# Kernel tuning notes

Measured on AMD Instinct MI355X. Metric: run time of the kernel, lower is better.

The kernel has to match this reference:

```python
import jax, jax.numpy as jnp
import numpy as np

N, IN, HID, OUT, HD = 512, 256, 256, 256, 64  # n_agents, in_dim, hid_dim, out_dim, head_dim (out_dim // n_heads)


def _mlp2(x, w1, b1, w2, b2):
    return jax.nn.relu(x @ w1.T + b1) @ w2.T + b2


def setup_inputs():
    key = jax.random.key(0)
    ks = jax.random.split(key, 32)
    p = lambda i, shape: jax.random.normal(ks[i], shape, dtype=jnp.float32) * 0.05
    V = jax.random.normal(ks[0], (N, IN), dtype=jnp.float32)
    adj = jax.random.randint(ks[1], (N, N), 0, 2, dtype=jnp.int32)
    adj = adj.at[jnp.arange(N), jnp.arange(N)].set(1)  # self-loops so no softmax row is all -inf
    prev_hidden = jax.random.normal(ks[2], (N, HID), dtype=jnp.float32)
    return {
        "V": V, "adj": adj, "prev_hidden": prev_hidden,
        "W1": p(3, (HID, IN)), "sa0": p(4, (HID,)), "sa1": p(5, (HID,)),
        "ce_w1": p(6, (HID, 2 * IN)), "ce_b1": p(7, (HID,)), "ce_w2": p(8, (HD, HID)), "ce_b2": p(9, (HD,)),
        "ca0": p(10, (HD,)), "ca1": p(11, (HD,)),
        "te_w1": p(12, (HID, IN + HID)), "te_b1": p(13, (HID,)), "te_w2": p(14, (HD, HID)), "te_b2": p(15, (HD,)),
        "ta0": p(16, (HD,)), "ta1": p(17, (HD,)),
        "pe_w1": p(18, (HID, 3 * IN)), "pe_b1": p(19, (HID,)), "pe_w2": p(20, (HD, HID)), "pe_b2": p(21, (HD,)),
        "pa0": p(22, (HD,)), "pa1": p(23, (HD,)),
        "W2": p(24, (OUT, HID + 2 * HD + 1)), "op_w": p(25, (OUT, OUT)), "op_b": p(26, (OUT,)),
        "ln_g": jnp.ones((OUT,), jnp.float32), "ln_b": jnp.zeros((OUT,), jnp.float32),
    }


def _forward(V, adj, prev_hidden, W1, sa0, sa1, ce_w1, ce_b1, ce_w2, ce_b2, ca0, ca1,
             te_w1, te_b1, te_w2, te_b2, ta0, ta1, pe_w1, pe_b1, pe_w2, pe_b2, pa0, pa1,
             W2, op_w, op_b, ln_g, ln_b):
    neg = -jnp.inf
    # --- branch 1: standard GAT attention ---
    Wh1 = V @ W1.T                                             # (N, HID)
    s1 = (Wh1 @ sa0)[:, None] + (Wh1 @ sa1)[None, :]           # (N, N)
    s1 = jnp.where(adj == 0, neg, s1)
    H1 = jax.nn.softmax(s1, axis=1) @ Wh1                      # (N, HID)
    # --- branch 2: causal, all ordered pairs i != j ---
    wA, wB = ce_w1[:, :IN], ce_w1[:, IN:]
    h = jax.nn.relu((V @ wA.T)[:, None, :] + (V @ wB.T)[None, :, :] + ce_b1)  # (N, N, HID)
    f = h @ ce_w2.T + ce_b2                                    # (N, N, HD)
    s2 = jnp.where(jnp.eye(N, dtype=bool), neg, f @ (ca0 + ca1))
    a2 = jax.nn.softmax(s2.reshape(-1)).reshape(N, N)          # softmax over all off-diagonal pairs
    H2 = jnp.broadcast_to(jnp.einsum('ij,ijd->d', a2, f), (N, HD))
    # --- branch 3: temporal; (N,1) scores broadcast against (N,N) causal mask ---
    tf = _mlp2(jnp.concatenate([V, prev_hidden], -1), te_w1, te_b1, te_w2, te_b2)  # (N, HD)
    ts = tf @ (ta0 + ta1)                                      # (N,)
    cmask = jnp.triu(jnp.ones((N, N), dtype=bool), 1)
    s3 = jnp.where(cmask, neg, jnp.broadcast_to(ts[:, None], (N, N)))
    H3 = jax.nn.softmax(s3, axis=1) @ tf                       # (N, HD) == prefix means of tf
    # --- branch 4: cooperative; first two neighbors in index order (zeros if < 2) ---
    pos = jnp.where(adj == 1, jnp.arange(N)[None, :], N)
    srt = jnp.sort(pos, axis=1)
    i0, i1 = srt[:, 0], srt[:, 1]
    valid = (i1 < N)[:, None]
    n0 = jnp.where(valid, V[jnp.clip(i0, 0, N - 1)], 0.0)
    n1 = jnp.where(valid, V[jnp.clip(i1, 0, N - 1)], 0.0)
    cf = _mlp2(jnp.concatenate([V, n0, n1], -1), pe_w1, pe_b1, pe_w2, pe_b2)  # (N, HD)
    # torch: softmax over dim of size 1 -> all ones, alpha^T @ cf == column sums -> (HD,)
    # then unsqueezed to (HD,1) and zero-padded to (N,1) since HD < N  (faithful to source bug)
    H4v = cf.sum(axis=0)
    H4 = jnp.concatenate([H4v, jnp.zeros((N - HD,), V.dtype)])[:, None]       # (N, 1)
    # --- combine ---
    Hc = jnp.concatenate([H1, H2, H3, H4], axis=-1) @ W2.T     # (N, OUT)
    out = Hc @ op_w.T + op_b
    mu = out.mean(-1, keepdims=True)
    var = ((out - mu) ** 2).mean(-1, keepdims=True)
    y = (out - mu) / jnp.sqrt(var + 1e-5) * ln_g + ln_b        # LayerNorm, eps=1e-5
    return jax.nn.elu(y)                                       # dropout is identity in eval


def reference(V, adj, prev_hidden, W1, sa0, sa1, ce_w1, ce_b1, ce_w2, ce_b2, ca0, ca1,
              te_w1, te_b1, te_w2, te_b2, ta0, ta1, pe_w1, pe_b1, pe_w2, pe_b2, pa0, pa1,
              W2, op_w, op_b, ln_g, ln_b):
    return _forward(V, adj, prev_hidden, W1, sa0, sa1, ce_w1, ce_b1, ce_w2, ce_b2, ca0, ca1,
                    te_w1, te_b1, te_w2, te_b2, ta0, ta1, pe_w1, pe_b1, pe_w2, pe_b2, pa0, pa1,
                    W2, op_w, op_b, ln_g, ln_b)
```

## Files before the change

### kernel.cpp

```cpp
#include <hip/hip_runtime.h>

typedef unsigned short u16;

constexpr int kN   = 512;
constexpr int kIN  = 256;
constexpr int kHID = 256;
constexpr int kHD  = 64;
constexpr int kOUT = 256;

__device__ __forceinline__ float us2f(u16 u){
  union { unsigned int i; float f; } c; c.i = ((unsigned int)u) << 16; return c.f;
}
__device__ __forceinline__ u16 f2us(float f){
  union { float f; unsigned int i; } c; c.f = f;
  unsigned int r = c.i + 0x7fff + ((c.i >> 16) & 1);
  return (u16)(r >> 16);
}
__device__ __forceinline__ float ldraw(const void* p, size_t i, bool f32){
  return f32 ? ((const float*)p)[i] : us2f(((const u16*)p)[i]);
}

__device__ bool probe_is_f32(const unsigned int* __restrict__ V){
  __shared__ int cnt;
  if (threadIdx.x == 0) cnt = 0;
  __syncthreads();
  int c = 0;
  for (int k = threadIdx.x; k < 4096; k += 256){
    float x = us2f((u16)(V[k] & 0xffffu));
    if (!(fabsf(x) <= 32.0f)) c++;
  }
  atomicAdd(&cnt, c);
  __syncthreads();
  return cnt > 64;
}

__device__ __forceinline__ float blk_red(float v, float* tmp, bool isMax){
  int lane = threadIdx.x & 63, wv = threadIdx.x >> 6;
  #pragma unroll
  for (int o = 32; o > 0; o >>= 1){
    float t = __shfl_down(v, o, 64);
    v = isMax ? fmaxf(v, t) : (v + t);
  }
  __syncthreads();
  if (lane == 0) tmp[wv] = v;
  __syncthreads();
  float r = tmp[0];
  for (int i = 1; i < 4; ++i) r = isMax ? fmaxf(r, tmp[i]) : (r + tmp[i]);
  return r;
}

constexpr int kNConv = 22;
struct ConvArgs { const void* src[kNConv]; float* dst[kNConv]; int n[kNConv]; };
struct GSeg2 { const float* X; const float* W; float* C; int ldx, ldw, ldc, K;
               const float* bias; int act; };
struct GS32 { const float* X; const float* W; float* C; int ldx, ldw, ldc, K; int bkn; };

struct Args {
  const unsigned int* Vraw;
  const int* adj;
  const void* rprev;
  int* flag; void* out;
  const void *rca0,*rca1,*rcw2,*rcb2,*rtw2,*rpw2;
  float *Vf,*W1f,*sa1f,*cw1f,*cb1f,*cw2f,*cb2f,*ca0f,*ca1f;
  float *tw1f,*tb1f,*tw2f,*tb2f,*pw1f,*pb1f,*pw2f,*pb2f;
  float *W2f,*opwf,*opbf,*lngf,*lnbf;
  float *tw2t,*pw2t,*Wcomb,*OM,*ow4;
  float *Wh1,*e1v,*wadj,*Hc,*Am,*Bm,*uvec,*beta;
  float *s2,*maxp,*zp,*MZ,*gsum;
  float *hidden_t,*hidden_p,*tfm,*cfm,*H4v,*Xp,*Xt,*out3;
  ConvArgs ca;
  GSeg2 gs[5];
};

__device__ __forceinline__ void gemm32_body(const GS32 sg, int tm, int tn, int tid,
                                            float* Xs, float* Ws)
{
  const int i0 = tm << 5, n0 = tn << 5;
  const int xrow = tid >> 3;
  const int xk = (tid & 7) << 2;
  const int rg = (tid >> 4) << 1;
  const int cg = (tid & 15) << 1;
  const float* Xb = sg.X + (size_t)i0 * sg.ldx;
  const float* Wb = sg.bkn ? (sg.W + n0) : (sg.W + (size_t)n0 * sg.ldw);
  float4 xr, wr;
  auto loadT = [&](int kt){
    xr = *(const float4*)(Xb + (size_t)xrow * sg.ldx + kt + xk);
    if (sg.bkn) wr = *(const float4*)(Wb + (size_t)(kt + xrow) * sg.ldw + xk);
    else        wr = *(const float4*)(Wb + (size_t)xrow * sg.ldw + kt + xk);
  };
  auto writeT = [&](int bu){
    float* xs = Xs + bu*1152;
    xs[(xk+0)*36 + xrow] = xr.x; xs[(xk+1)*36 + xrow] = xr.y;
    xs[(xk+2)*36 + xrow] = xr.z; xs[(xk+3)*36 + xrow] = xr.w;
    float* wsp = Ws + bu*1152;
    if (sg.bkn){
      wsp[xrow*36 + xk+0] = wr.x; wsp[xrow*36 + xk+1] = wr.y;
      wsp[xrow*36 + xk+2] = wr.z; wsp[xrow*36 + xk+3] = wr.w;
    } else {
      wsp[(xk+0)*36 + xrow] = wr.x; wsp[(xk+1)*36 + xrow] = wr.y;
      wsp[(xk+2)*36 + xrow] = wr.z; wsp[(xk+3)*36 + xrow] = wr.w;
    }
  };
  loadT(0); writeT(0); __syncthreads();
  float a00=0,a01=0,a10=0,a11=0;
  const int nkt = sg.K >> 5;
  for (int t = 0; t < nkt; ++t){
    if (t+1 < nkt) loadT((t+1) << 5);
    const float* xs = Xs + (t&1)*1152;
    const float* wsp = Ws + (t&1)*1152;
    #pragma unroll
    for (int kk = 0; kk < 32; ++kk){
      float2 av = *(const float2*)&xs[kk*36 + rg];
      float2 bv = *(const float2*)&wsp[kk*36 + cg];
      a00 += av.x*bv.x; a01 += av.x*bv.y;
      a10 += av.y*bv.x; a11 += av.y*bv.y;
    }
    if (t+1 < nkt) writeT((t+1)&1);
    __syncthreads();
  }
  float* cp = sg.C + (size_t)(i0+rg)*sg.ldc + n0 + cg;
  *(float2*)cp = make_float2(a00, a01);
  *(float2*)(cp + sg.ldc) = make_float2(a10, a11);
}

__device__ void body_gemmA(const Args& A, int it, int tid, char* SM)
{
  float (*Xs)[32][68] = (float (*)[32][68])SM;
  float (*Ws)[32][68] = (float (*)[32][68])(SM + 17408);
  int seg = it >> 5, x = it & 31;
  const GSeg2 sg = A.gs[seg];
  const int tm = x & 7, tn = x >> 3;
  const int i0 = tm << 6, n0 = tn << 6;

  const int xrow = tid >> 3;
  const int xk   = (tid & 7) << 2;
  const int rg = (tid >> 4) << 2;
  const int cg = (tid & 15) << 2;

  const float* Xb = sg.X + (size_t)i0 * sg.ldx;
  const float* Wb = sg.W + (size_t)n0 * sg.ldw;

  float4 xr0, xr1, wr0, wr1;
  auto loadT = [&](int kt){
    xr0 = *(const float4*)(Xb + (size_t)xrow * sg.ldx + kt + xk);
    xr1 = *(const float4*)(Xb + (size_t)(xrow+32) * sg.ldx + kt + xk);
    wr0 = *(const float4*)(Wb + (size_t)xrow * sg.ldw + kt + xk);
    wr1 = *(const float4*)(Wb + (size_t)(xrow+32) * sg.ldw + kt + xk);
  };
  auto writeT = [&](int bu){
    Xs[bu][xk+0][xrow] = xr0.x;  Xs[bu][xk+1][xrow] = xr0.y;
    Xs[bu][xk+2][xrow] = xr0.z;  Xs[bu][xk+3][xrow] = xr0.w;
    Xs[bu][xk+0][xrow+32] = xr1.x;  Xs[bu][xk+1][xrow+32] = xr1.y;
    Xs[bu][xk+2][xrow+32] = xr1.z;  Xs[bu][xk+3][xrow+32] = xr1.w;
    Ws[bu][xk+0][xrow]    = wr0.x; Ws[bu][xk+1][xrow]    = wr0.y;
    Ws[bu][xk+2][xrow]    = wr0.z; Ws[bu][xk+3][xrow]    = wr0.w;
    Ws[bu][xk+0][xrow+32] = wr1.x; Ws[bu][xk+1][xrow+32] = wr1.y;
    Ws[bu][xk+2][xrow+32] = wr1.z; Ws[bu][xk+3][xrow+32] = wr1.w;
  };

  loadT(0); writeT(0); __syncthreads();

  float acc[4][4] = {};
  const int nkt = sg.K >> 5;
  for (int t = 0; t < nkt; ++t){
    if (t + 1 < nkt) loadT((t + 1) << 5);
    const int bu = t & 1;
    #pragma unroll
    for (int kk = 0; kk < 32; ++kk){
      const float4 av = *(const float4*)&Xs[bu][kk][rg];
      const float4 bv = *(const float4*)&Ws[bu][kk][cg];
      acc[0][0]+=av.x*bv.x; acc[0][1]+=av.x*bv.y; acc[0][2]+=av.x*bv.z; acc[0][3]+=av.x*bv.w;
      acc[1][0]+=av.y*bv.x; acc[1][1]+=av.y*bv.y; acc[1][2]+=av.y*bv.z; acc[1][3]+=av.y*bv.w;
      acc[2][0]+=av.z*bv.x; acc[2][1]+=av.z*bv.y; acc[2][2]+=av.z*bv.z; acc[2][3]+=av.z*bv.w;
      acc[3][0]+=av.w*bv.x; acc[3][1]+=av.w*bv.y; acc[3][2]+=av.w*bv.z; acc[3][3]+=av.w*bv.w;
    }
    if (t + 1 < nkt) writeT((t + 1) & 1);
    __syncthreads();
  }

  float bb[4] = {0.f, 0.f, 0.f, 0.f};
  if (sg.bias){
    bb[0] = sg.bias[n0+cg+0]; bb[1] = sg.bias[n0+cg+1];
    bb[2] = sg.bias[n0+cg+2]; bb[3] = sg.bias[n0+cg+3];
  }
  #pragma unroll
  for (int ri = 0; ri < 4; ++ri){
    float4 v = make_float4(acc[ri][0]+bb[0], acc[ri][1]+bb[1],
                           acc[ri][2]+bb[2], acc[ri][3]+bb[3]);
    if (sg.act){
      v.x = fmaxf(v.x, 0.f); v.y = fmaxf(v.y, 0.f);
      v.z = fmaxf(v.z, 0.f); v.w = fmaxf(v.w, 0.f);
    }
    *(float4*)(sg.C + (size_t)(i0 + rg + ri) * sg.ldc + (n0 + cg)) = v;
  }

  if (seg == 0){
    int cb = n0 + cg;
    float s0 = A.sa1f[cb], s1 = A.sa1f[cb+1], s2v = A.sa1f[cb+2], s3 = A.sa1f[cb+3];
    #pragma unroll
    for (int ri = 0; ri < 4; ++ri){
      float v = acc[ri][0]*s0 + acc[ri][1]*s1 + acc[ri][2]*s2v + acc[ri][3]*s3;
      v += __shfl_xor(v, 1, 16);
      v += __shfl_xor(v, 2, 16);
      v += __shfl_xor(v, 4, 16);
      v += __shfl_xor(v, 8, 16);
      if ((tid & 15) == 0) atomicAdd(&A.e1v[i0 + rg + ri], v);
    }
  }
}

__global__ __launch_bounds__(256) void k_s0(Args A)
{
  __shared__ __align__(16) char SM[16896];
  int it = blockIdx.x, tid = threadIdx.x;
  bool f32 = probe_is_f32(A.Vraw);
  if (it < 256){
    if (it == 0){
      if (tid == 0) *A.flag = f32 ? 1 : 0;
      A.e1v[tid] = 0.f; A.e1v[tid + 256] = 0.f;
    }
    int t = it*256 + tid;
    for (int s = 0; s < kNConv; ++s){
      int n4 = A.ca.n[s] >> 2;
      float4* d = (float4*)A.ca.dst[s];
      if (f32){
        const float4* sf = (const float4*)A.ca.src[s];
        for (int i = t; i < n4; i += 65536) d[i] = sf[i];
      } else {
        const ushort4* sb = (const ushort4*)A.ca.src[s];
        for (int i = t; i < n4; i += 65536){
          ushort4 u = sb[i];
          d[i] = make_float4(us2f(u.x), us2f(u.y), us2f(u.z), us2f(u.w));
        }
      }
    }
  } else if (it < 768){
    unsigned long long* msk = (unsigned long long*)SM;
    int* sj = (int*)(SM + 64);
    int i = it - 256;
    int w = tid >> 6, lane = tid & 63;
    unsigned long long m0 = __ballot(A.adj[(size_t)i*kN + tid] != 0);
    unsigned long long m1 = __ballot(A.adj[(size_t)i*kN + 256 + tid] != 0);
    if (lane == 0){ msk[w] = m0; msk[4 + w] = m1; }
    __syncthreads();
    if (tid == 0){
      int j0 = -1, j1 = -1;
      for (int c = 0; c < 8 && j1 < 0; ++c){
        unsigned long long m = msk[c];
        while (m && j1 < 0){
          int bb = __builtin_ctzll(m);
          int j = c*64 + bb;
          if (j0 < 0) j0 = j; else j1 = j;
          m &= m - 1;
        }
      }
      if (j1 < 0) j0 = -1;
      sj[0] = j0; sj[1] = j1;
    }
    __syncthreads();
    int j0 = sj[0], j1 = sj[1];
    float vi = ldraw(A.Vraw, (size_t)i*kIN + tid, f32);
    A.Xp[(size_t)i*768 + tid]       = vi;
    A.Xp[(size_t)i*768 + 256 + tid] = (j0 >= 0) ? ldraw(A.Vraw, (size_t)j0*kIN + tid, f32) : 0.f;
    A.Xp[(size_t)i*768 + 512 + tid] = (j1 >= 0) ? ldraw(A.Vraw, (size_t)j1*kIN + tid, f32) : 0.f;
    A.Xt[(size_t)i*512 + tid]       = vi;
    A.Xt[(size_t)i*512 + 256 + tid] = ldraw(A.rprev, (size_t)i*kHID + tid, f32);
  } else if (it == 768){
    float* st = (float*)SM;
    if (tid < 64){ st[tid] = ldraw(A.rca0, tid, f32) + ldraw(A.rca1, tid, f32); A.H4v[tid] = 0.f; }
    __syncthreads();
    float a = 0.f;
    for (int d = 0; d < kHD; ++d) a += ldraw(A.rcw2, (size_t)d*kHID + tid, f32) * st[d];
    A.uvec[tid] = a;
    if (tid == 0){
      float b = 0.f;
      for (int d = 0; d < kHD; ++d) b += ldraw(A.rcb2, d, f32) * st[d];
      *A.beta = b;
    }
  } else {
    const void* src = (it == 769) ? A.rtw2 : A.rpw2;
    float* dst = (it == 769) ? A.tw2t : A.pw2t;
    float* st = (float*)SM;
    for (int ch = 0; ch < 4; ++ch){
      __syncthreads();
      #pragma unroll
      for (int e = 0; e < 16; ++e){
        int lin = e*256 + tid, r = lin >> 6, c = lin & 63;
        st[r*65 + c] = ldraw(src, (size_t)r*256 + ch*64 + c, f32);
      }
      __syncthreads();
      #pragma unroll
      for (int e = 0; e < 16; ++e){
        int lin = e*256 + tid, kc = lin >> 6, dd = lin & 63;
        dst[(size_t)(ch*64 + kc)*64 + dd] = st[dd*65 + kc];
      }
    }
  }
}

__global__ __launch_bounds__(256) void k_s1(Args A)
{
  __shared__ __align__(16) char SM[34816];
  int it = blockIdx.x, tid = threadIdx.x;
  if (it < 160){
    body_gemmA(A, it, tid, SM);
  } else if (it < 240){
    int q = it - 160, tm = q & 7, tn = q >> 3;
    const float* Wsrc = A.W2f + ((tn < 8) ? 0 : 64);
    GS32 sg{A.opwf, Wsrc, A.Wcomb, 256, 385, 320, 256, 1};
    gemm32_body(sg, tm, tn, tid, (float*)SM, (float*)(SM + 9216));
  } else if (it < 256){
    int q = it - 240;
    GS32 sg{A.opwf, A.W2f + 256, A.OM, 256, 385, 64, 256, 1};
    gemm32_body(sg, q & 7, q >> 3, tid, (float*)SM, (float*)(SM + 9216));
  } else {
    float* st = (float*)SM;
    st[tid] = A.W2f[(size_t)tid*385 + 384];
    __syncthreads();
    float a = 0.f;
    const float* orow = A.opwf + (size_t)tid*256;
    for (int m = 0; m < 256; m += 4){
      float4 o4 = *(const float4*)(orow + m);
      a += o4.x*st[m] + o4.y*st[m+1] + o4.z*st[m+2] + o4.w*st[m+3];
    }
    A.ow4[tid] = a;
  }
}

__global__ __launch_bounds__(256) void k_s2(Args A)
{
  __shared__ __align__(16) float SM2[4*256 + 256];
  int it = blockIdx.x, tid = threadIdx.x;
  if (it < 512){
    int i = it;
    int m0 = A.adj[(size_t)i*kN + tid];
    int m1 = A.adj[(size_t)i*kN + tid + 256];
    float ea = A.e1v[tid], eb = A.e1v[tid+256];
    float v0 = m0 ? ea : -1e30f;
    float v1 = m1 ? eb : -1e30f;
    float m = blk_red(fmaxf(v0, v1), SM2, true);
    float z = blk_red((m0 ? expf(ea-m) : 0.f) + (m1 ? expf(eb-m) : 0.f), SM2, false);
    float iz = 1.0f / z;
    A.wadj[(size_t)i*kN + tid]       = m0 ? expf(ea - m) * iz : 0.f;
    A.wadj[(size_t)i*kN + tid + 256] = m1 ? expf(eb - m) * iz : 0.f;
  } else if (it < 1536){
    float* aib = SM2;
    float* uu  = SM2 + 1024;
    int q = it - 512;
    int i0 = (q & 127) * 4, j0 = (q >> 7) * 64;
    int wv = tid >> 6, lane = tid & 63;
    uu[tid] = A.uvec[tid];
    float b1v = A.cb1f[tid];
    #pragma unroll
    for (int r = 0; r < 4; ++r) aib[r*256 + tid] = A.Am[(size_t)(i0+r)*kHID + tid] + b1v;
    __syncthreads();
    int i = i0 + wv, j = j0 + lane;
    const float4* bp = (const float4*)(A.Bm + (size_t)j*kHID);
    float acc = *A.beta;
    #pragma unroll 8
    for (int k4 = 0; k4 < kHID/4; ++k4){
      float4 bv = bp[k4];
      float4 a4 = *(const float4*)&aib[wv*256 + k4*4];
      float4 u4 = *(const float4*)&uu[k4*4];
      acc += fmaxf(a4.x+bv.x,0.f)*u4.x + fmaxf(a4.y+bv.y,0.f)*u4.y
           + fmaxf(a4.z+bv.z,0.f)*u4.z + fmaxf(a4.w+bv.w,0.f)*u4.w;
    }
    if (j == i) acc = -1e30f;
    A.s2[(size_t)i*kN + j] = acc;
    float m = acc;
    #pragma unroll
    for (int o = 32; o > 0; o >>= 1) m = fmaxf(m, __shfl_down(m, o, 64));
    m = __shfl(m, 0, 64);
    float e = expf(acc - m);
    #pragma unroll
    for (int o = 32; o > 0; o >>= 1) e += __shfl_down(e, o, 64);
    if (lane == 0){
      int pb = q*4 + wv;
      A.maxp[pb] = m; A.zp[pb] = e;
    }
  } else {
    int q = it - 1536;
    int m = q >> 5, grp = q & 31;
    const float* X  = m ? A.hidden_p : A.hidden_t;
    const float* Wt = m ? A.pw2t : A.tw2t;
    const float* bi = m ? A.pb2f : A.tb2f;
    float* C = m ? A.cfm : A.tfm;
    int i0 = grp*16 + (tid >> 6)*4;
    int d = tid & 63;
    const float* x0 = X + (size_t)i0*256;
    const float* x1 = x0 + 256;
    const float* x2 = x0 + 512;
    const float* x3 = x0 + 768;
    float a0=0.f, a1=0.f, a2=0.f, a3=0.f;
    for (int k = 0; k < 256; k += 4){
      float w0 = Wt[(size_t)(k+0)*64 + d];
      float w1 = Wt[(size_t)(k+1)*64 + d];
      float w2 = Wt[(size_t)(k+2)*64 + d];
      float w3 = Wt[(size_t)(k+3)*64 + d];
      float4 f0 = *(const float4*)(x0 + k);
      float4 f1 = *(const float4*)(x1 + k);
      float4 f2 = *(const float4*)(x2 + k);
      float4 f3 = *(const float4*)(x3 + k);
      a0 += f0.x*w0 + f0.y*w1 + f0.z*w2 + f0.w*w3;
      a1 += f1.x*w0 + f1.y*w1 + f1.z*w2 + f1.w*w3;
      a2 += f2.x*w0 + f2.y*w1 + f2.z*w2 + f2.w*w3;
      a3 += f3.x*w0 + f3.y*w1 + f3.z*w2 + f3.w*w3;
    }
    float bd = bi[d];
    C[(size_t)(i0+0)*64 + d] = a0 + bd;
    C[(size_t)(i0+1)*64 + d] = a1 + bd;
    C[(size_t)(i0+2)*64 + d] = a2 + bd;
    C[(size_t)(i0+3)*64 + d] = a3 + bd;
  }
}

__global__ __launch_bounds__(256) void k_s3(Args A)
{
  __shared__ __align__(16) char SM[18432];
  int it = blockIdx.x, tid = threadIdx.x;
  if (it < 128){
    GS32 sg{A.wadj, A.Wh1, A.Hc, 512, 256, 320, 512, 1};
    gemm32_body(sg, it & 15, it >> 4, tid, (float*)SM, (float*)(SM + 9216));
  } else if (it < 192){
    int d = it - 128;
    int lane = tid & 63, wv = tid >> 6;
    float v0 = A.tfm[(size_t)(2*tid)*kHD + d];
    float v1 = A.tfm[(size_t)(2*tid+1)*kHD + d];
    float s = v0 + v1;
    float x = s;
    #pragma unroll
    for (int off = 1; off < 64; off <<= 1){
      float y = __shfl_up(x, off, 64);
      if (lane >= off) x += y;
    }
    float* wsum = (float*)SM;
    if (lane == 63) wsum[wv] = x;
    __syncthreads();
    float base = 0.f;
    for (int k = 0; k < wv; ++k) base += wsum[k];
    float excl = base + x - s;
    A.Hc[(size_t)(2*tid)*320 + 256 + d]   = (excl + v0) / (float)(2*tid + 1);
    A.Hc[(size_t)(2*tid+1)*320 + 256 + d] = (excl + s)  / (float)(2*tid + 2);
  } else if (it < 200){
    float* sm = (float*)SM;
    int d = tid & 63, sub = tid >> 6;
    int r0 = (it-192)*64 + sub*16;
    float s = 0.f;
    #pragma unroll
    for (int e = 0; e < 16; ++e) s += A.cfm[(size_t)(r0+e)*kHD + d];
    sm[sub*64 + d] = s;
    __syncthreads();
    if (tid < 64)
      atomicAdd(&A.H4v[tid], sm[tid] + sm[64+tid] + sm[128+tid] + sm[192+tid]);
  } else {
    float* red = (float*)SM;
    float m = -1e30f;
    #pragma unroll
    for (int r = 0; r < 16; ++r) m = fmaxf(m, A.maxp[tid + 256*r]);
    m = blk_red(m, red, true);
    float z = 0.f;
    #pragma unroll
    for (int r = 0; r < 16; ++r) z += A.zp[tid + 256*r] * expf(A.maxp[tid + 256*r] - m);
    z = blk_red(z, red, false);
    if (tid == 0){ A.MZ[0] = m; A.MZ[1] = z; }
    A.gsum[tid] = 0.f;
  }
}

__global__ __launch_bounds__(256) void k_s4(Args A)
{
  __shared__ __align__(16) char SM[18432];
  int it = blockIdx.x, tid = threadIdx.x;
  if (it < 1024){
    float* wt = (float*)SM;
    int i0 = (it & 31) * 16, j0 = (it >> 5) * 16;
    float M = A.MZ[0], invZ = 1.0f / A.MZ[1];
    {
      int r = tid >> 4, c = tid & 15;
      wt[r*16 + c] = expf(A.s2[(size_t)(i0+r)*kN + (j0+c)] - M) * invZ;
    }
    float b1v = A.cb1f[tid];
    float aib[16];
    #pragma unroll
    for (int r = 0; r < 16; ++r) aib[r] = A.Am[(size_t)(i0+r)*kHID + tid] + b1v;
    __syncthreads();
    float acc = 0.f;
    for (int j = 0; j < 16; ++j){
      float bj = A.Bm[(size_t)(j0+j)*kHID + tid];
      #pragma unroll
      for (int r = 0; r < 16; ++r)
        acc += wt[r*16 + j] * fmaxf(aib[r] + bj, 0.f);
    }
    atomicAdd(&A.gsum[tid], acc);
  } else {
    int q = it - 1024;
    GS32 sg{A.Hc, A.Wcomb, A.out3, 320, 320, 256, 320, 0};
    gemm32_body(sg, q & 15, q >> 4, tid, (float*)SM, (float*)(SM + 9216));
  }
}

__global__ __launch_bounds__(256) void k_s5(Args A)
{
  __shared__ float gs[kHID];
  __shared__ float part[kHD][4];
  __shared__ float h2s[kHD];
  __shared__ float cc2s[kOUT];
  int b = blockIdx.x, tid = threadIdx.x;
  bool f32 = (*A.flag != 0);
  gs[tid] = A.gsum[tid];
  __syncthreads();
  {
    int dd = tid >> 2, q = tid & 3;
    float a = 0.f;
    for (int kk = 0; kk < 64; ++kk){
      int k = q*64 + kk;
      a += gs[k] * A.cw2f[(size_t)dd*kHID + k];
    }
    part[dd][q] = a;
  }
  __syncthreads();
  if (tid < kHD)
    h2s[tid] = A.cb2f[tid] + part[tid][0] + part[tid][1] + part[tid][2] + part[tid][3];
  __syncthreads();
  {
    float a = 0.f;
    const float* om = A.OM + (size_t)tid*64;
    for (int d = 0; d < kHD; d += 4){
      float4 o4 = *(const float4*)(om + d);
      a += o4.x*h2s[d] + o4.y*h2s[d+1] + o4.z*h2s[d+2] + o4.w*h2s[d+3];
    }
    cc2s[tid] = a;
  }
  __syncthreads();
  int row = b*4 + (tid >> 6), lane = tid & 63;
  float h4r = (row < kHD) ? A.H4v[row] : 0.f;
  float4 v  = *(const float4*)(A.out3 + (size_t)row*kOUT + lane*4);
  float4 c2 = *(const float4*)(&cc2s[lane*4]);
  float4 o4 = *(const float4*)(A.ow4 + lane*4);
  float4 pb = *(const float4*)(A.opbf + lane*4);
  v.x += c2.x + h4r*o4.x + pb.x;
  v.y += c2.y + h4r*o4.y + pb.y;
  v.z += c2.z + h4r*o4.z + pb.z;
  v.w += c2.w + h4r*o4.w + pb.w;
  float s = v.x + v.y + v.z + v.w;
  #pragma unroll
  for (int o = 32; o > 0; o >>= 1) s += __shfl_xor(s, o, 64);
  float mu = s * (1.0f/kOUT);
  float dx = v.x-mu, dy = v.y-mu, dz = v.z-mu, dw = v.w-mu;
  float ss = dx*dx + dy*dy + dz*dz + dw*dw;
  #pragma unroll
  for (int o = 32; o > 0; o >>= 1) ss += __shfl_xor(ss, o, 64);
  float rs = rsqrtf(ss * (1.0f/kOUT) + 1e-5f);
  float4 g  = *(const float4*)(A.lngf + lane*4);
  float4 be = *(const float4*)(A.lnbf + lane*4);
  float y0 = dx*rs*g.x + be.x, y1 = dy*rs*g.y + be.y;
  float y2 = dz*rs*g.z + be.z, y3 = dw*rs*g.w + be.w;
  y0 = (y0 > 0.f) ? y0 : expm1f(y0);
  y1 = (y1 > 0.f) ? y1 : expm1f(y1);
  y2 = (y2 > 0.f) ? y2 : expm1f(y2);
  y3 = (y3 > 0.f) ? y3 : expm1f(y3);
  if (f32){
    *(float4*)((float*)A.out + (size_t)row*kOUT + lane*4) = make_float4(y0,y1,y2,y3);
  } else {
    ushort4 u; u.x = f2us(y0); u.y = f2us(y1); u.z = f2us(y2); u.w = f2us(y3);
    ((ushort4*)A.out)[(size_t)row*64 + lane] = u;
  }
}

extern "C" void kernel_launch(void* const* d_in, const int* in_sizes, int n_in,
                              void* d_out, int out_size, void* d_ws, size_t ws_size,
                              hipStream_t stream)
{
  const void* V     = d_in[0];
  const int*  adj   = (const int*)d_in[1];
  const void* prev  = d_in[2];
  const void* W1    = d_in[3];
  const void* sa1   = d_in[5];
  const void* ce_w1 = d_in[6];
  const void* ce_b1 = d_in[7];
  const void* ce_w2 = d_in[8];
  const void* ce_b2 = d_in[9];
  const void* ca0   = d_in[10];
  const void* ca1   = d_in[11];
  const void* te_w1 = d_in[12];
  const void* te_b1 = d_in[13];
  const void* te_w2 = d_in[14];
  const void* te_b2 = d_in[15];
  const void* pe_w1 = d_in[18];
  const void* pe_b1 = d_in[19];
  const void* pe_w2 = d_in[20];
  const void* pe_b2 = d_in[21];
  const void* W2    = d_in[24];
  const void* op_w  = d_in[25];
  const void* op_b  = d_in[26];
  const void* ln_g  = d_in[27];
  const void* ln_b  = d_in[28];

  float* ws  = (float*)d_ws;
  int*  flag = (int*)ws;
  float* p   = ws + 16;
  float* Vf   = p; p += 131072;
  float* W1f  = p; p += 65536;
  float* sa1f = p; p += 256;
  float* cw1f = p; p += 131072;
  float* cb1f = p; p += 256;
  float* cw2f = p; p += 16384;
  float* cb2f = p; p += 64;
  float* ca0f = p; p += 64;
  float* ca1f = p; p += 64;
  float* tw1f = p; p += 131072;
  float* tb1f = p; p += 256;
  float* tw2f = p; p += 16384;
  float* tb2f = p; p += 64;
  float* pw1f = p; p += 196608;
  float* pb1f = p; p += 256;
  float* pw2f = p; p += 16384;
  float* pb2f = p; p += 64;
  float* W2f  = p; p += 98560;
  float* opwf = p; p += 65536;
  float* opbf = p; p += 256;
  float* lngf = p; p += 256;
  float* lnbf = p; p += 256;
  float* tw2t = p; p += 16384;
  float* pw2t = p; p += 16384;
  float* Wcomb= p; p += 81920;
  float* OM   = p; p += 16384;
  float* ow4  = p; p += 256;
  float* Wh1      = p; p += 131072;
  float* e1v      = p; p += 512;
  float* wadj     = p; p += 262144;
  float* Hc       = p; p += 163840;
  float* Am       = p; p += 131072;
  float* Bm       = p; p += 131072;
  float* uvec     = p; p += 256;
  float* beta     = p; p += 16;
  float* s2       = p; p += 262144;
  float* maxp     = p; p += 4096;
  float* zpart    = p; p += 4096;
  float* MZ       = p; p += 16;
  float* gsum     = p; p += 256;
  float* hidden_t = p; p += 131072;
  float* hidden_p = p; p += 131072;
  float* tfm      = p; p += 32768;
  float* cfm      = p; p += 32768;
  float* H4v      = p; p += 64;
  float* Xp       = p; p += 393216;
  float* Xt       = p; p += 262144;
  float* out3     = p; p += 131072;

  Args A;
  A.Vraw = (const unsigned int*)V; A.adj = adj; A.rprev = prev;
  A.flag = flag; A.out = d_out;
  A.rca0 = ca0; A.rca1 = ca1; A.rcw2 = ce_w2; A.rcb2 = ce_b2; A.rtw2 = te_w2; A.rpw2 = pe_w2;
  A.Vf=Vf; A.W1f=W1f; A.sa1f=sa1f; A.cw1f=cw1f; A.cb1f=cb1f;
  A.cw2f=cw2f; A.cb2f=cb2f; A.ca0f=ca0f; A.ca1f=ca1f;
  A.tw1f=tw1f; A.tb1f=tb1f; A.tw2f=tw2f; A.tb2f=tb2f;
  A.pw1f=pw1f; A.pb1f=pb1f; A.pw2f=pw2f; A.pb2f=pb2f;
  A.W2f=W2f; A.opwf=opwf; A.opbf=opbf; A.lngf=lngf; A.lnbf=lnbf;
  A.tw2t=tw2t; A.pw2t=pw2t; A.Wcomb=Wcomb; A.OM=OM; A.ow4=ow4;
  A.Wh1=Wh1; A.e1v=e1v; A.wadj=wadj; A.Hc=Hc;
  A.Am=Am; A.Bm=Bm; A.uvec=uvec; A.beta=beta;
  A.s2=s2; A.maxp=maxp; A.zp=zpart; A.MZ=MZ; A.gsum=gsum;
  A.hidden_t=hidden_t; A.hidden_p=hidden_p;
  A.tfm=tfm; A.cfm=cfm; A.H4v=H4v; A.Xp=Xp; A.Xt=Xt; A.out3=out3;

  {
    const void* srcs[kNConv] = {V, W1, sa1, ce_w1, ce_b1, ce_w2, ce_b2, ca0, ca1,
                                te_w1, te_b1, te_w2, te_b2, pe_w1, pe_b1, pe_w2, pe_b2,
                                W2, op_w, op_b, ln_g, ln_b};
    float* dsts[kNConv] = {Vf, W1f, sa1f, cw1f, cb1f, cw2f, cb2f, ca0f, ca1f,
                           tw1f, tb1f, tw2f, tb2f, pw1f, pb1f, pw2f, pb2f,
                           W2f, opwf, opbf, lngf, lnbf};
    int ns[kNConv] = {131072, 65536, 256, 131072, 256, 16384, 64, 64, 64,
                      131072, 256, 16384, 64, 196608, 256, 16384, 64,
                      98560, 65536, 256, 256, 256};
    for (int s = 0; s < kNConv; ++s){ A.ca.src[s] = srcs[s]; A.ca.dst[s] = dsts[s]; A.ca.n[s] = ns[s]; }
  }
  A.gs[0] = {Vf, W1f,        Wh1,      256, 256, 256, 256, nullptr, 0};
  A.gs[1] = {Vf, cw1f,       Am,       256, 512, 256, 256, nullptr, 0};
  A.gs[2] = {Vf, cw1f + 256, Bm,       256, 512, 256, 256, nullptr, 0};
  A.gs[3] = {Xt, tw1f,       hidden_t, 512, 512, 256, 512, tb1f, 1};
  A.gs[4] = {Xp, pw1f,       hidden_p, 768, 768, 256, 768, pb1f, 1};

  k_s0<<<771,  256, 0, stream>>>(A);
  k_s1<<<257,  256, 0, stream>>>(A);
  k_s2<<<1600, 256, 0, stream>>>(A);
  k_s3<<<201,  256, 0, stream>>>(A);
  k_s4<<<1152, 256, 0, stream>>>(A);
  k_s5<<<128,  256, 0, stream>>>(A);
}
```

Baseline: 262.3 us.

## Split hidden GEMMs by K into partials, add reduce pass, restructure causal scores

The K=512 and K=768 hidden-layer GEMMs become K=256 partial GEMMs, one per input segment, so all segments share one shape and balance better across blocks. A new elementwise pass sums the partials and applies bias and ReLU. The causal pairwise score computation is rewritten so each thread block handles 128 columns per tile, using a wave-wide reduction over the hidden dimension instead of a per-lane loop. The cost is extra partial buffers, an additional kernel launch, and more global memory traffic for the partial sums.

```diff
diff --git a/kernel.cpp b/kernel.cpp
--- a/kernel.cpp
+++ b/kernel.cpp
@@ -49,27 +49,26 @@
   return r;
 }
 
-constexpr int kNConv = 22;
+constexpr int kNConv = 23;
 struct ConvArgs { const void* src[kNConv]; float* dst[kNConv]; int n[kNConv]; };
-struct GSeg2 { const float* X; const float* W; float* C; int ldx, ldw, ldc, K;
-               const float* bias; int act; };
+struct GSeg2 { const float* X; const float* W; float* C; int ldx, ldw, ldc, K; };
 struct GS32 { const float* X; const float* W; float* C; int ldx, ldw, ldc, K; int bkn; };
 
 struct Args {
   const unsigned int* Vraw;
   const int* adj;
-  const void* rprev;
   int* flag; void* out;
   const void *rca0,*rca1,*rcw2,*rcb2,*rtw2,*rpw2;
-  float *Vf,*W1f,*sa1f,*cw1f,*cb1f,*cw2f,*cb2f,*ca0f,*ca1f;
+  float *Vf,*prevf,*W1f,*sa1f,*cw1f,*cb1f,*cw2f,*cb2f,*ca0f,*ca1f;
   float *tw1f,*tb1f,*tw2f,*tb2f,*pw1f,*pb1f,*pw2f,*pb2f;
   float *W2f,*opwf,*opbf,*lngf,*lnbf;
   float *tw2t,*pw2t,*Wcomb,*OM,*ow4;
   float *Wh1,*e1v,*wadj,*Hc,*Am,*Bm,*uvec,*beta;
   float *s2,*maxp,*zp,*MZ,*gsum;
-  float *hidden_t,*hidden_p,*tfm,*cfm,*H4v,*Xp,*Xt,*out3;
+  float *htp0,*htp1,*hpp0,*hpp1,*hpp2,*hidden_t,*hidden_p;
+  float *tfm,*cfm,*H4v,*Xp,*out3;
   ConvArgs ca;
-  GSeg2 gs[5];
+  GSeg2 gs[8];
 };
 
 __device__ __forceinline__ void gemm32_body(const GS32 sg, int tm, int tn, int tid,
@@ -178,21 +177,10 @@
     __syncthreads();
   }
 
-  float bb[4] = {0.f, 0.f, 0.f, 0.f};
-  if (sg.bias){
-    bb[0] = sg.bias[n0+cg+0]; bb[1] = sg.bias[n0+cg+1];
-    bb[2] = sg.bias[n0+cg+2]; bb[3] = sg.bias[n0+cg+3];
-  }
   #pragma unroll
-  for (int ri = 0; ri < 4; ++ri){
-    float4 v = make_float4(acc[ri][0]+bb[0], acc[ri][1]+bb[1],
-                           acc[ri][2]+bb[2], acc[ri][3]+bb[3]);
-    if (sg.act){
-      v.x = fmaxf(v.x, 0.f); v.y = fmaxf(v.y, 0.f);
-      v.z = fmaxf(v.z, 0.f); v.w = fmaxf(v.w, 0.f);
-    }
-    *(float4*)(sg.C + (size_t)(i0 + rg + ri) * sg.ldc + (n0 + cg)) = v;
-  }
+  for (int ri = 0; ri < 4; ++ri)
+    *(float4*)(sg.C + (size_t)(i0 + rg + ri) * sg.ldc + (n0 + cg)) =
+      make_float4(acc[ri][0], acc[ri][1], acc[ri][2], acc[ri][3]);
 
   if (seg == 0){
     int cb = n0 + cg;
@@ -259,12 +247,9 @@
     }
     __syncthreads();
     int j0 = sj[0], j1 = sj[1];
-    float vi = ldraw(A.Vraw, (size_t)i*kIN + tid, f32);
-    A.Xp[(size_t)i*768 + tid]       = vi;
+    A.Xp[(size_t)i*768 + tid]       = ldraw(A.Vraw, (size_t)i*kIN + tid, f32);
     A.Xp[(size_t)i*768 + 256 + tid] = (j0 >= 0) ? ldraw(A.Vraw, (size_t)j0*kIN + tid, f32) : 0.f;
     A.Xp[(size_t)i*768 + 512 + tid] = (j1 >= 0) ? ldraw(A.Vraw, (size_t)j1*kIN + tid, f32) : 0.f;
-    A.Xt[(size_t)i*512 + tid]       = vi;
-    A.Xt[(size_t)i*512 + 256 + tid] = ldraw(A.rprev, (size_t)i*kHID + tid, f32);
   } else if (it == 768){
     float* st = (float*)SM;
     if (tid < 64){ st[tid] = ldraw(A.rca0, tid, f32) + ldraw(A.rca1, tid, f32); A.H4v[tid] = 0.f; }
@@ -302,15 +287,15 @@
 {
   __shared__ __align__(16) char SM[34816];
   int it = blockIdx.x, tid = threadIdx.x;
-  if (it < 160){
+  if (it < 256){
     body_gemmA(A, it, tid, SM);
-  } else if (it < 240){
-    int q = it - 160, tm = q & 7, tn = q >> 3;
+  } else if (it < 336){
+    int q = it - 256, tm = q & 7, tn = q >> 3;
     const float* Wsrc = A.W2f + ((tn < 8) ? 0 : 64);
     GS32 sg{A.opwf, Wsrc, A.Wcomb, 256, 385, 320, 256, 1};
     gemm32_body(sg, tm, tn, tid, (float*)SM, (float*)(SM + 9216));
-  } else if (it < 256){
-    int q = it - 240;
+  } else if (it < 352){
+    int q = it - 336;
     GS32 sg{A.opwf, A.W2f + 256, A.OM, 256, 385, 64, 256, 1};
     gemm32_body(sg, q & 7, q >> 3, tid, (float*)SM, (float*)(SM + 9216));
   } else {
@@ -329,10 +314,28 @@
 
 __global__ __launch_bounds__(256) void k_s2(Args A)
 {
-  __shared__ __align__(16) float SM2[4*256 + 256];
+  __shared__ float SM2[8];
   int it = blockIdx.x, tid = threadIdx.x;
-  if (it < 512){
-    int i = it;
+  if (it < 128){
+    int f = it*256 + tid;
+    int c4 = f & 63;
+    {
+      float4 a = ((const float4*)A.htp0)[f], bb = ((const float4*)A.htp1)[f];
+      float4 bi = ((const float4*)A.tb1f)[c4];
+      ((float4*)A.hidden_t)[f] = make_float4(
+        fmaxf(a.x+bb.x+bi.x,0.f), fmaxf(a.y+bb.y+bi.y,0.f),
+        fmaxf(a.z+bb.z+bi.z,0.f), fmaxf(a.w+bb.w+bi.w,0.f));
+    }
+    {
+      float4 a = ((const float4*)A.hpp0)[f], bb = ((const float4*)A.hpp1)[f];
+      float4 c = ((const float4*)A.hpp2)[f];
+      float4 bi = ((const float4*)A.pb1f)[c4];
+      ((float4*)A.hidden_p)[f] = make_float4(
+        fmaxf(a.x+bb.x+c.x+bi.x,0.f), fmaxf(a.y+bb.y+c.y+bi.y,0.f),
+        fmaxf(a.z+bb.z+c.z+bi.z,0.f), fmaxf(a.w+bb.w+c.w+bi.w,0.f));
+    }
+  } else {
+    int i = it - 128;
     int m0 = A.adj[(size_t)i*kN + tid];
     int m1 = A.adj[(size_t)i*kN + tid + 256];
     float ea = A.e1v[tid], eb = A.e1v[tid+256];
@@ -343,44 +346,15 @@
     float iz = 1.0f / z;
     A.wadj[(size_t)i*kN + tid]       = m0 ? expf(ea - m) * iz : 0.f;
     A.wadj[(size_t)i*kN + tid + 256] = m1 ? expf(eb - m) * iz : 0.f;
-  } else if (it < 1536){
-    float* aib = SM2;
-    float* uu  = SM2 + 1024;
-    int q = it - 512;
-    int i0 = (q & 127) * 4, j0 = (q >> 7) * 64;
-    int wv = tid >> 6, lane = tid & 63;
-    uu[tid] = A.uvec[tid];
-    float b1v = A.cb1f[tid];
-    #pragma unroll
-    for (int r = 0; r < 4; ++r) aib[r*256 + tid] = A.Am[(size_t)(i0+r)*kHID + tid] + b1v;
-    __syncthreads();
-    int i = i0 + wv, j = j0 + lane;
-    const float4* bp = (const float4*)(A.Bm + (size_t)j*kHID);
-    float acc = *A.beta;
-    #pragma unroll 8
-    for (int k4 = 0; k4 < kHID/4; ++k4){
-      float4 bv = bp[k4];
-      float4 a4 = *(const float4*)&aib[wv*256 + k4*4];
-      float4 u4 = *(const float4*)&uu[k4*4];
-      acc += fmaxf(a4.x+bv.x,0.f)*u4.x + fmaxf(a4.y+bv.y,0.f)*u4.y
-           + fmaxf(a4.z+bv.z,0.f)*u4.z + fmaxf(a4.w+bv.w,0.f)*u4.w;
-    }
-    if (j == i) acc = -1e30f;
-    A.s2[(size_t)i*kN + j] = acc;
-    float m = acc;
-    #pragma unroll
-    for (int o = 32; o > 0; o >>= 1) m = fmaxf(m, __shfl_down(m, o, 64));
-    m = __shfl(m, 0, 64);
-    float e = expf(acc - m);
-    #pragma unroll
-    for (int o = 32; o > 0; o >>= 1) e += __shfl_down(e, o, 64);
-    if (lane == 0){
-      int pb = q*4 + wv;
-      A.maxp[pb] = m; A.zp[pb] = e;
-    }
-  } else {
-    int q = it - 1536;
-    int m = q >> 5, grp = q & 31;
+  }
+}
+
+__global__ __launch_bounds__(256) void k_s3(Args A)
+{
+  __shared__ __align__(16) float SM3[4*256 + 256];
+  int it = blockIdx.x, tid = threadIdx.x;
+  if (it < 64){
+    int m = it >> 5, grp = it & 31;
     const float* X  = m ? A.hidden_p : A.hidden_t;
     const float* Wt = m ? A.pw2t : A.tw2t;
     const float* bi = m ? A.pb2f : A.tb2f;
@@ -411,10 +385,64 @@
     C[(size_t)(i0+1)*64 + d] = a1 + bd;
     C[(size_t)(i0+2)*64 + d] = a2 + bd;
     C[(size_t)(i0+3)*64 + d] = a3 + bd;
-  }
-}
-
-__global__ __launch_bounds__(256) void k_s3(Args A)
+  } else {
+    float* aib = SM3;
+    float* uu  = SM3 + 1024;
+    int q = it - 64;
+    int i0 = (q & 127) * 4, jt = q >> 7;
+    int w = tid >> 6, lane = tid & 63;
+    uu[tid] = A.uvec[tid];
+    float b1v = A.cb1f[tid];
+    #pragma unroll
+    for (int r = 0; r < 4; ++r) aib[r*256 + tid] = A.Am[(size_t)(i0+r)*kHID + tid] + b1v;
+    __syncthreads();
+    float bet = *A.beta;
+    float4 u4 = *(const float4*)&uu[lane*4];
+    float4 a4[4];
+    #pragma unroll
+    for (int r = 0; r < 4; ++r) a4[r] = *(const float4*)&aib[r*256 + lane*4];
+    float sv[4] = {-1e30f, -1e30f, -1e30f, -1e30f};
+    int jbase = jt*128 + w*32;
+    for (int jj = 0; jj < 32; ++jj){
+      int j = jbase + jj;
+      float4 bv = *(const float4*)(A.Bm + (size_t)j*kHID + lane*4);
+      #pragma unroll
+      for (int r = 0; r < 4; ++r){
+        float p = fmaxf(a4[r].x+bv.x,0.f)*u4.x + fmaxf(a4[r].y+bv.y,0.f)*u4.y
+                + fmaxf(a4[r].z+bv.z,0.f)*u4.z + fmaxf(a4[r].w+bv.w,0.f)*u4.w;
+        #pragma unroll
+        for (int o = 32; o > 0; o >>= 1) p += __shfl_xor(p, o, 64);
+        p += bet;
+        if (j == i0 + r) p = -1e30f;
+        if (lane == jj) sv[r] = p;
+      }
+    }
+    float lmax = -1e30f;
+    if (lane < 32){
+      #pragma unroll
+      for (int r = 0; r < 4; ++r){
+        A.s2[(size_t)(i0+r)*kN + jbase + lane] = sv[r];
+        lmax = fmaxf(lmax, sv[r]);
+      }
+    }
+    float m = lmax;
+    #pragma unroll
+    for (int o = 32; o > 0; o >>= 1) m = fmaxf(m, __shfl_xor(m, o, 64));
+    float z = 0.f;
+    if (lane < 32){
+      #pragma unroll
+      for (int r = 0; r < 4; ++r) z += expf(sv[r] - m);
+    }
+    #pragma unroll
+    for (int o = 32; o > 0; o >>= 1) z += __shfl_xor(z, o, 64);
+    if (lane == 0){
+      int pb = q*4 + w;
+      A.maxp[pb] = m; A.zp[pb] = z;
+    }
+  }
+}
+
+__global__ __launch_bounds__(256) void k_s4(Args A)
 {
   __shared__ __align__(16) char SM[18432];
   int it = blockIdx.x, tid = threadIdx.x;
@@ -456,18 +484,18 @@
     float* red = (float*)SM;
     float m = -1e30f;
     #pragma unroll
-    for (int r = 0; r < 16; ++r) m = fmaxf(m, A.maxp[tid + 256*r]);
+    for (int r = 0; r < 8; ++r) m = fmaxf(m, A.maxp[tid + 256*r]);
     m = blk_red(m, red, true);
     float z = 0.f;
     #pragma unroll
-    for (int r = 0; r < 16; ++r) z += A.zp[tid + 256*r] * expf(A.maxp[tid + 256*r] - m);
+    for (int r = 0; r < 8; ++r) z += A.zp[tid + 256*r] * expf(A.maxp[tid + 256*r] - m);
     z = blk_red(z, red, false);
     if (tid == 0){ A.MZ[0] = m; A.MZ[1] = z; }
     A.gsum[tid] = 0.f;
   }
 }
 
-__global__ __launch_bounds__(256) void k_s4(Args A)
+__global__ __launch_bounds__(256) void k_s5(Args A)
 {
   __shared__ __align__(16) char SM[18432];
   int it = blockIdx.x, tid = threadIdx.x;
@@ -499,7 +527,7 @@
   }
 }
 
-__global__ __launch_bounds__(256) void k_s5(Args A)
+__global__ __launch_bounds__(256) void k_s6(Args A)
 {
   __shared__ float gs[kHID];
   __shared__ float part[kHD][4];
@@ -600,6 +628,7 @@
   int*  flag = (int*)ws;
   float* p   = ws + 16;
   float* Vf   = p; p += 131072;
+  float* prevf= p; p += 131072;
   float* W1f  = p; p += 65536;
   float* sa1f = p; p += 256;
   float* cw1f = p; p += 131072;
@@ -639,20 +668,24 @@
   float* zpart    = p; p += 4096;
   float* MZ       = p; p += 16;
   float* gsum     = p; p += 256;
+  float* htp0     = p; p += 131072;
+  float* htp1     = p; p += 131072;
+  float* hpp0     = p; p += 131072;
+  float* hpp1     = p; p += 131072;
+  float* hpp2     = p; p += 131072;
   float* hidden_t = p; p += 131072;
   float* hidden_p = p; p += 131072;
   float* tfm      = p; p += 32768;
   float* cfm      = p; p += 32768;
   float* H4v      = p; p += 64;
   float* Xp       = p; p += 393216;
-  float* Xt       = p; p += 262144;
   float* out3     = p; p += 131072;
 
   Args A;
-  A.Vraw = (const unsigned int*)V; A.adj = adj; A.rprev = prev;
+  A.Vraw = (const unsigned int*)V; A.adj = adj;
   A.flag = flag; A.out = d_out;
   A.rca0 = ca0; A.rca1 = ca1; A.rcw2 = ce_w2; A.rcb2 = ce_b2; A.rtw2 = te_w2; A.rpw2 = pe_w2;
-  A.Vf=Vf; A.W1f=W1f; A.sa1f=sa1f; A.cw1f=cw1f; A.cb1f=cb1f;
+  A.Vf=Vf; A.prevf=prevf; A.W1f=W1f; A.sa1f=sa1f; A.cw1f=cw1f; A.cb1f=cb1f;
   A.cw2f=cw2f; A.cb2f=cb2f; A.ca0f=ca0f; A.ca1f=ca1f;
   A.tw1f=tw1f; A.tb1f=tb1f; A.tw2f=tw2f; A.tb2f=tb2f;
   A.pw1f=pw1f; A.pb1f=pb1f; A.pw2f=pw2f; A.pb2f=pb2f;
@@ -661,31 +694,36 @@
   A.Wh1=Wh1; A.e1v=e1v; A.wadj=wadj; A.Hc=Hc;
   A.Am=Am; A.Bm=Bm; A.uvec=uvec; A.beta=beta;
   A.s2=s2; A.maxp=maxp; A.zp=zpart; A.MZ=MZ; A.gsum=gsum;
+  A.htp0=htp0; A.htp1=htp1; A.hpp0=hpp0; A.hpp1=hpp1; A.hpp2=hpp2;
   A.hidden_t=hidden_t; A.hidden_p=hidden_p;
-  A.tfm=tfm; A.cfm=cfm; A.H4v=H4v; A.Xp=Xp; A.Xt=Xt; A.out3=out3;
+  A.tfm=tfm; A.cfm=cfm; A.H4v=H4v; A.Xp=Xp; A.out3=out3;
 
   {
-    const void* srcs[kNConv] = {V, W1, sa1, ce_w1, ce_b1, ce_w2, ce_b2, ca0, ca1,
+    const void* srcs[kNConv] = {V, prev, W1, sa1, ce_w1, ce_b1, ce_w2, ce_b2, ca0, ca1,
                                 te_w1, te_b1, te_w2, te_b2, pe_w1, pe_b1, pe_w2, pe_b2,
                                 W2, op_w, op_b, ln_g, ln_b};
-    float* dsts[kNConv] = {Vf, W1f, sa1f, cw1f, cb1f, cw2f, cb2f, ca0f, ca1f,
+    float* dsts[kNConv] = {Vf, prevf, W1f, sa1f, cw1f, cb1f, cw2f, cb2f, ca0f, ca1f,
                            tw1f, tb1f, tw2f, tb2f, pw1f, pb1f, pw2f, pb2f,
                            W2f, opwf, opbf, lngf, lnbf};
-    int ns[kNConv] = {131072, 65536, 256, 131072, 256, 16384, 64, 64, 64,
+    int ns[kNConv] = {131072, 131072, 65536, 256, 131072, 256, 16384, 64, 64, 64,
                       131072, 256, 16384, 64, 196608, 256, 16384, 64,
                       98560, 65536, 256, 256, 256};
     for (int s = 0; s < kNConv; ++s){ A.ca.src[s] = srcs[s]; A.ca.dst[s] = dsts[s]; A.ca.n[s] = ns[s]; }
   }
-  A.gs[0] = {Vf, W1f,        Wh1,      256, 256, 256, 256, nullptr, 0};
-  A.gs[1] = {Vf, cw1f,       Am,       256, 512, 256, 256, nullptr, 0};
-  A.gs[2] = {Vf, cw1f + 256, Bm,       256, 512, 256, 256, nullptr, 0};
-  A.gs[3] = {Xt, tw1f,       hidden_t, 512, 512, 256, 512, tb1f, 1};
-  A.gs[4] = {Xp, pw1f,       hidden_p, 768, 768, 256, 768, pb1f, 1};
+  A.gs[0] = {Vf,       W1f,        Wh1,  256, 256, 256, 256};
+  A.gs[1] = {Vf,       cw1f,       Am,   256, 512, 256, 256};
+  A.gs[2] = {Vf,       cw1f + 256, Bm,   256, 512, 256, 256};
+  A.gs[3] = {Vf,       tw1f,       htp0, 256, 512, 256, 256};
+  A.gs[4] = {prevf,    tw1f + 256, htp1, 256, 512, 256, 256};
+  A.gs[5] = {Xp,       pw1f,       hpp0, 768, 768, 256, 256};
+  A.gs[6] = {Xp + 256, pw1f + 256, hpp1, 768, 768, 256, 256};
+  A.gs[7] = {Xp + 512, pw1f + 512, hpp2, 768, 768, 256, 256};
 
   k_s0<<<771,  256, 0, stream>>>(A);
-  k_s1<<<257,  256, 0, stream>>>(A);
-  k_s2<<<1600, 256, 0, stream>>>(A);
-  k_s3<<<201,  256, 0, stream>>>(A);
-  k_s4<<<1152, 256, 0, stream>>>(A);
-  k_s5<<<128,  256, 0, stream>>>(A);
-}
+  k_s1<<<353,  256, 0, stream>>>(A);
+  k_s2<<<640,  256, 0, stream>>>(A);
+  k_s3<<<576,  256, 0, stream>>>(A);
+  k_s4<<<201,  256, 0, stream>>>(A);
+  k_s5<<<1152, 256, 0, stream>>>(A);
+  k_s6<<<128,  256, 0, stream>>>(A);
+}
```

Result: faster. 254.6 us (-2.9%).
